# Optimization experiments

Measured on AMD Instinct MI355X. Metric: run time of the kernel, lower is better.

## Reference

```python
import jax, jax.numpy as jnp
import numpy as np

N_NODES = 100000
N_EDGES = 1600000
N_GRAPHS = 64
D = 128


def gcn_conv(x, W, b, src, dst, num_nodes):
    # PyG GCNConv: x' = D^{-1/2} (A + I) D^{-1/2} (X W) + b
    h = x @ W  # [N, H]
    deg = jax.ops.segment_sum(jnp.ones_like(dst, dtype=h.dtype), dst,
                              num_segments=num_nodes)  # includes self-loop (>=1)
    dinv = jax.lax.rsqrt(deg)
    norm = dinv[src] * dinv[dst]  # [E+N]
    msg = h[src] * norm[:, None]  # gather + scale
    out = jax.ops.segment_sum(msg, dst, num_segments=num_nodes)
    return out + b


def setup_inputs() -> dict:
    key = jax.random.key(0)
    ks = jax.random.split(key, 10)
    x = jax.random.normal(ks[0], (N_NODES, D), dtype=jnp.float32)
    edge_index = jax.random.randint(ks[1], (2, N_EDGES), 0, N_NODES, dtype=jnp.int64)
    batch = jnp.sort(jax.random.randint(ks[2], (N_NODES,), 0, N_GRAPHS, dtype=jnp.int64))
    s = 1.0 / np.sqrt(D)
    W1 = jax.random.normal(ks[3], (D, D), dtype=jnp.float32) * s
    b1 = jnp.zeros((D,), dtype=jnp.float32)
    W2 = jax.random.normal(ks[4], (D, D), dtype=jnp.float32) * s
    b2 = jnp.zeros((D,), dtype=jnp.float32)
    Wfc = jax.random.normal(ks[5], (D, D), dtype=jnp.float32) * s
    bfc = jnp.zeros((D,), dtype=jnp.float32)
    return {"x": x, "edge_index": edge_index, "batch": batch,
            "W1": W1, "b1": b1, "W2": W2, "b2": b2, "Wfc": Wfc, "bfc": bfc}


def reference(x, edge_index, batch, W1, b1, W2, b2, Wfc, bfc):
    num_nodes = x.shape[0]
    # add self-loops (PyG default add_self_loops=True)
    loop = jnp.arange(num_nodes, dtype=edge_index.dtype)
    src = jnp.concatenate([edge_index[0], loop])
    dst = jnp.concatenate([edge_index[1], loop])

    h = jax.nn.relu(gcn_conv(x, W1, b1, src, dst, num_nodes))
    h = jax.nn.relu(gcn_conv(h, W2, b2, src, dst, num_nodes))

    # global_mean_pool over graph segment ids
    sums = jax.ops.segment_sum(h, batch, num_segments=N_GRAPHS)
    cnts = jax.ops.segment_sum(jnp.ones((num_nodes,), h.dtype), batch,
                               num_segments=N_GRAPHS)
    pooled = sums / jnp.maximum(cnts, 1.0)[:, None]

    return jax.nn.relu(pooled @ Wfc + bfc)
```

## Files before the change

### kernel.cpp

```cpp
#include <hip/hip_runtime.h>
#include <hip/hip_bf16.h>
#include <stdint.h>

typedef unsigned int uint;
typedef unsigned short ushort;
typedef __attribute__((ext_vector_type(8))) short short8;
typedef __attribute__((ext_vector_type(4))) float floatx4;

#define DD 128
#define BSHIFT 9
#define NBLK 256

__device__ __forceinline__ float bf2f(ushort h){ return __uint_as_float(((uint)h)<<16); }
__device__ __forceinline__ ushort f2bf(float f){
    uint u = __float_as_uint(f);
    u += 0x7fffu + ((u>>16)&1u);
    return (ushort)(u>>16);
}

__global__ void k_detect(const int* ei, const ushort* x, const ushort* W1, int* flags){
    int t = threadIdx.x;
    unsigned long long b0 = __ballot((t < 32) ? (ei[2*t+1] == 0) : 1);
    uint ex = (((uint)x[2*t])  >> 7) & 0xffu;
    uint ew = (((uint)W1[2*t]) >> 7) & 0xffu;
    unsigned long long b1 = __ballot(ex >= 90u && ex <= 160u);
    unsigned long long b2 = __ballot(ew >= 90u && ew <= 160u);
    if (t == 0){
        flags[0] = (b0 == ~0ull) ? 1 : 0;
        flags[1] = (__popcll(b1) >= 48) ? 1 : 0;
        flags[2] = (__popcll(b2) >= 48) ? 1 : 0;
    }
}

__global__ void k_canon(const void* s0,const void* s1,const void* s2,
                        const void* s3,const void* s4,const void* s5,
                        float* d0,float* d1,float* d2,float* d3,float* d4,float* d5,
                        ushort* wb1, ushort* wb2,
                        const int* flags){
    int f = flags[2];
    int i = blockIdx.x*blockDim.x + threadIdx.x;
    const void* s; float* d; int off; int r;
    if (i < 49152){
        r = i>>14; off = i & 16383;
        s = (r==0)?s0:((r==1)?s1:s2);
        d = (r==0)?d0:((r==1)?d1:d2);
    } else {
        int j = i - 49152; r = j>>7; off = j & 127;
        if (r >= 3) return;
        s = (r==0)?s3:((r==1)?s4:s5);
        d = (r==0)?d3:((r==1)?d4:d5);
        d[off] = f ? bf2f(((const ushort*)s)[off]) : ((const float*)s)[off];
        return;
    }
    float val = f ? bf2f(((const ushort*)s)[off]) : ((const float*)s)[off];
    d[off] = val;
    if (r < 2){
        int k = off>>7, n = off&127;
        int c = n>>4, nn = n&15, kk = k>>5, q = (k>>3)&3, j = k&7;
        ushort* wb = (r==0) ? wb1 : wb2;
        wb[((c*4+kk)*64 + q*16 + nn)*8 + j] = f2bf(val);
    }
}

__global__ void k_init(float* pooled, int PM, int* buktot, int nbuk){
    int i = blockIdx.x*blockDim.x + threadIdx.x;
    if (i < PM) pooled[i] = 0.f;
    if (i < nbuk) buktot[i] = 0;
}

__global__ __launch_bounds__(256) void k_hist(const int* __restrict__ ei,
                                              const int* __restrict__ flags,
                                              int* __restrict__ ghist,
                                              int* __restrict__ buktot,
                                              int E, int nbuk, int chunk){
    __shared__ int lh[1024];
    int f = flags[0];
    int t = threadIdx.x, b = blockIdx.x;
    for (int i=t;i<nbuk;i+=256) lh[i]=0;
    __syncthreads();
    int e0 = b*chunk, e1 = min(E, e0+chunk);
    for (int e=e0+t; e<e1; e+=256){
        int d = f ? ei[2*(E+e)] : ei[E+e];
        atomicAdd(&lh[d>>BSHIFT],1);
    }
    __syncthreads();
    for (int i=t;i<nbuk;i+=256){
        int v = lh[i];
        ghist[i*NBLK + b] = v;
        if (v) atomicAdd(&buktot[i], v);
    }
}

__global__ void k_scanB2(const int* __restrict__ buktot, int* __restrict__ bukoff, int nbuk){
    __shared__ int ts[256];
    int t = threadIdx.x;
    int v = (t<nbuk) ? buktot[t] : 0;
    ts[t] = v; __syncthreads();
    for (int off=1; off<256; off<<=1){
        int x = (t>=off) ? ts[t-off] : 0;
        __syncthreads(); ts[t] += x; __syncthreads();
    }
    if (t<nbuk) bukoff[t] = ts[t] - v;
}

__global__ __launch_bounds__(256) void k_apply(const int* __restrict__ ghist,
                                               const int* __restrict__ bukoff,
                                               int* __restrict__ gstart, int nbuk){
    __shared__ int ts[256];
    int b = blockIdx.x, t = threadIdx.x;
    int v = ghist[b*NBLK + t];
    ts[t] = v; __syncthreads();
    for (int off=1; off<256; off<<=1){
        int x = (t>=off) ? ts[t-off] : 0;
        __syncthreads(); ts[t] += x; __syncthreads();
    }
    gstart[b*NBLK + t] = bukoff[b] + ts[t] - v;
}

__global__ __launch_bounds__(256) void k_scat(const int* __restrict__ ei,
                                              const int* __restrict__ flags,
                                              const int* __restrict__ gstart,
                                              uint2* __restrict__ pairs,
                                              int E, int nbuk, int chunk){
    __shared__ int cur[1024];
    int f = flags[0];
    int t = threadIdx.x, b = blockIdx.x;
    for (int i=t;i<nbuk;i+=256) cur[i] = gstart[i*NBLK + b];
    __syncthreads();
    int e0 = b*chunk, e1 = min(E, e0+chunk);
    for (int e=e0+t; e<e1; e+=256){
        int d = f ? ei[2*(E+e)] : ei[E+e];
        int s = f ? ei[2*e]     : ei[e];
        int p = atomicAdd(&cur[d>>BSHIFT],1);
        pairs[p] = make_uint2((uint)s,(uint)d);
    }
}

__global__ __launch_bounds__(256) void k_build(const uint2* __restrict__ pairs,
                                               const int* __restrict__ gstart,
                                               int* __restrict__ rowptr,
                                               float* __restrict__ dinv,
                                               int* __restrict__ srcb,
                                               int E, int nbuk, int M){
    __shared__ int cnt[512], off[512], cur[512], ps[256];
    int b = blockIdx.x, t = threadIdx.x;
    int base = gstart[b*NBLK];
    int end  = (b+1<nbuk) ? gstart[(b+1)*NBLK] : E;
    for (int i=t;i<512;i+=256) cnt[i]=0;
    __syncthreads();
    for (int e=base+t; e<end; e+=256){
        uint2 pr = pairs[e];
        atomicAdd(&cnt[pr.y & 511],1);
    }
    __syncthreads();
    int c0 = cnt[2*t], c1 = cnt[2*t+1];
    int s = c0+c1;
    ps[t]=s; __syncthreads();
    for (int o2=1;o2<256;o2<<=1){
        int x=(t>=o2)?ps[t-o2]:0; __syncthreads(); ps[t]+=x; __syncthreads();
    }
    int ex = ps[t]-s;
    off[2*t]=ex;    off[2*t+1]=ex+c0;
    cur[2*t]=ex;    cur[2*t+1]=ex+c0;
    __syncthreads();
    for (int i=t;i<512;i+=256){
        int n = (b<<BSHIFT)+i;
        if (n<M){
            rowptr[n] = base + off[i];
            dinv[n]   = rsqrtf((float)(cnt[i]+1));
        }
    }
    if (b==0 && t==0) rowptr[M] = E;
    for (int e=base+t; e<end; e+=256){
        uint2 pr = pairs[e];
        int i = pr.y & 511;
        int p = atomicAdd(&cur[i],1);
        srcb[base+p] = (int)pr.x;
    }
}

__global__ __launch_bounds__(256) void k_gemm(const ushort* __restrict__ Xb,
                                              const float* __restrict__ Xf,
                                              const ushort* __restrict__ Wb,
                                              const float* __restrict__ dinv,
                                              const int* __restrict__ flags, int force_bf16,
                                              ushort* __restrict__ Hp, int M){
    __shared__ uint4 Xs4[1024];
    __shared__ uint4 Ws4[2048];
    int t = threadIdx.x;
    int n0 = blockIdx.x*64;
    int xbf = force_bf16 ? 1 : flags[1];

    {
        const uint4* sW = (const uint4*)Wb;
        #pragma unroll
        for (int j=0;j<8;j++) Ws4[t + j*256] = sW[t + j*256];
    }
    #pragma unroll
    for (int g=0; g<4; g++){
        int u = g*256 + t;
        int row = u>>4, kk = (u>>2)&3, q = u&3;
        int n = n0 + row;
        uint4 o;
        if (n < M){
            if (xbf){
                o = *(const uint4*)(Xb + (size_t)n*DD + kk*32 + q*8);
            } else {
                const float* p = Xf + (size_t)n*DD + kk*32 + q*8;
                float4 a = *(const float4*)p;
                float4 b = *(const float4*)(p+4);
                o.x = (uint)f2bf(a.x) | ((uint)f2bf(a.y)<<16);
                o.y = (uint)f2bf(a.z) | ((uint)f2bf(a.w)<<16);
                o.z = (uint)f2bf(b.x) | ((uint)f2bf(b.y)<<16);
                o.w = (uint)f2bf(b.z) | ((uint)f2bf(b.w)<<16);
            }
        } else { o = make_uint4(0,0,0,0); }
        int w = row>>4, m16 = row&15;
        Xs4[(w*4+kk)*64 + q*16 + m16] = o;
    }
    __syncthreads();

    int wv = t>>6, lane = t&63;
    const ushort* Xs = (const ushort*)Xs4;
    const ushort* Ws = (const ushort*)Ws4;

    floatx4 acc[8];
    #pragma unroll
    for (int c=0;c<8;c++) acc[c] = (floatx4){0.f,0.f,0.f,0.f};

    #pragma unroll
    for (int kk=0;kk<4;kk++){
        short8 af = *(const short8*)(Xs + ((size_t)((wv*4+kk)*64 + lane))*8);
        #pragma unroll
        for (int c=0;c<8;c++){
            short8 bf = *(const short8*)(Ws + ((size_t)((c*4+kk)*64 + lane))*8);
            acc[c] = __builtin_amdgcn_mfma_f32_16x16x32_bf16(af, bf, acc[c], 0, 0, 0);
        }
    }

    int quad = lane>>4, col = lane&15;
    int rbase = n0 + wv*16 + quad*4;
    float dv[4];
    #pragma unroll
    for (int r=0;r<4;r++) dv[r] = (rbase + r < M) ? dinv[rbase + r] : 0.f;
    #pragma unroll
    for (int c=0;c<8;c++){
        #pragma unroll
        for (int r=0;r<4;r++){
            int gn = rbase + r;
            if (gn < M) Hp[(size_t)gn*DD + c*16 + col] = f2bf(acc[c][r]*dv[r]);
        }
    }
}

__global__ __launch_bounds__(256) void k_gather(const ushort* __restrict__ Hp,
                                                const int* __restrict__ rowptr,
                                                const int* __restrict__ srcb,
                                                const float* __restrict__ dinv,
                                                const float* __restrict__ bc,
                                                ushort* __restrict__ Xout, int M){
    int wid  = (int)((blockIdx.x*(size_t)blockDim.x + threadIdx.x) >> 6);
    int lane = threadIdx.x & 63;
    if (wid >= M) return;
    const uint* Hp32 = (const uint*)Hp;

    uint v = Hp32[(size_t)wid*64 + lane];
    float a0 = __uint_as_float(v<<16);
    float a1 = __uint_as_float(v & 0xffff0000u);

    int rp  = rowptr[wid];
    int rp1 = rowptr[wid+1];
    while (rp < rp1){
        int m = rp1 - rp; if (m > 64) m = 64;
        int idx = (lane < m) ? srcb[rp + lane] : 0;
        int j = 0;
        for (; j+4 <= m; j += 4){
            int s0 = __shfl(idx, j,   64);
            int s1 = __shfl(idx, j+1, 64);
            int s2 = __shfl(idx, j+2, 64);
            int s3 = __shfl(idx, j+3, 64);
            uint u0 = Hp32[(size_t)s0*64 + lane];
            uint u1 = Hp32[(size_t)s1*64 + lane];
            uint u2 = Hp32[(size_t)s2*64 + lane];
            uint u3 = Hp32[(size_t)s3*64 + lane];
            a0 += __uint_as_float(u0<<16); a1 += __uint_as_float(u0&0xffff0000u);
            a0 += __uint_as_float(u1<<16); a1 += __uint_as_float(u1&0xffff0000u);
            a0 += __uint_as_float(u2<<16); a1 += __uint_as_float(u2&0xffff0000u);
            a0 += __uint_as_float(u3<<16); a1 += __uint_as_float(u3&0xffff0000u);
        }
        for (; j<m; j++){
            int s = __shfl(idx, j, 64);
            uint u = Hp32[(size_t)s*64 + lane];
            a0 += __uint_as_float(u<<16); a1 += __uint_as_float(u&0xffff0000u);
        }
        rp += m;
    }

    float w = dinv[wid];
    float o0 = fmaxf(fmaf(a0, w, bc[2*lane]),   0.f);
    float o1 = fmaxf(fmaf(a1, w, bc[2*lane+1]), 0.f);
    ((uint*)Xout)[(size_t)wid*64 + lane] = (uint)f2bf(o0) | ((uint)f2bf(o1)<<16);
}

__global__ __launch_bounds__(256) void k_pool(const ushort* __restrict__ X3,
                                              const int* __restrict__ batch,
                                              const int* __restrict__ flags,
                                              float* __restrict__ pooled, int M){
    int f = flags[0];
    int t = threadIdx.x;
    int c32 = t & 63;
    int row = t >> 6;
    int n0 = blockIdx.x * 256;
    if (n0 >= M) return;
    int nend = n0 + 256; if (nend > M) nend = M;
    const uint* X3u = (const uint*)X3;

    float a0 = 0.f, a1 = 0.f;
    int cur = -1;

    int n = n0 + row;
    #define POOL_PROC(gg, uu) \
        if ((gg) != cur){ \
            if (cur >= 0){ \
                atomicAdd(&pooled[cur*DD + 2*c32],   a0); \
                atomicAdd(&pooled[cur*DD + 2*c32+1], a1); \
            } \
            a0 = 0.f; a1 = 0.f; cur = (gg); \
        } \
        a0 += __uint_as_float((uu)<<16); \
        a1 += __uint_as_float((uu) & 0xffff0000u);

    for (; n + 12 < nend; n += 16){
        int g0 = f ? batch[2*n]      : batch[n];
        int g1 = f ? batch[2*(n+4)]  : batch[n+4];
        int g2 = f ? batch[2*(n+8)]  : batch[n+8];
        int g3 = f ? batch[2*(n+12)] : batch[n+12];
        uint u0 = X3u[(size_t)n*64      + c32];
        uint u1 = X3u[(size_t)(n+4)*64  + c32];
        uint u2 = X3u[(size_t)(n+8)*64  + c32];
        uint u3 = X3u[(size_t)(n+12)*64 + c32];
        POOL_PROC(g0, u0);
        POOL_PROC(g1, u1);
        POOL_PROC(g2, u2);
        POOL_PROC(g3, u3);
    }
    for (; n < nend; n += 4){
        int g = f ? batch[2*n] : batch[n];
        uint u = X3u[(size_t)n*64 + c32];
        POOL_PROC(g, u);
    }
    #undef POOL_PROC

    if (cur >= 0){
        atomicAdd(&pooled[cur*DD + 2*c32],   a0);
        atomicAdd(&pooled[cur*DD + 2*c32+1], a1);
    }
}

__global__ void k_cnt(const int* __restrict__ batch, const int* __restrict__ flags,
                      float* __restrict__ cntf, int M, int G){
    int f = flags[0];
    int g = blockIdx.x*blockDim.x + threadIdx.x;
    if (g >= G) return;
    int lo = 0, hi = M;
    while (lo < hi){ int mid = (lo+hi)>>1; int bv = f ? batch[2*mid] : batch[mid]; if (bv > g) hi = mid; else lo = mid+1; }
    int ub_g = lo;
    lo = 0; hi = M;
    while (lo < hi){ int mid = (lo+hi)>>1; int bv = f ? batch[2*mid] : batch[mid]; if (bv > g-1) hi = mid; else lo = mid+1; }
    cntf[g] = (float)(ub_g - lo);
}

__global__ void k_fc(const float* __restrict__ pooled, const float* __restrict__ cntf,
                     const float* __restrict__ Wcf, const float* __restrict__ bcf,
                     const int* __restrict__ flags, ushort* out16, float* out32){
    __shared__ float p[128];
    int g = blockIdx.x, c = threadIdx.x;
    p[c] = pooled[g*DD + c] / fmaxf(cntf[g], 1.f);
    __syncthreads();
    float acc = bcf[c];
    #pragma unroll 8
    for (int k=0;k<128;k++) acc = fmaf(p[k], Wcf[k*DD + c], acc);
    float r = fmaxf(acc, 0.f);
    if (flags[1]) out16[g*DD + c] = f2bf(r);
    else          out32[g*DD + c] = r;
}

extern "C" void kernel_launch(void* const* d_in, const int* in_sizes, int n_in,
                              void* d_out, int out_size, void* d_ws, size_t ws_size,
                              hipStream_t stream) {
    const void* x    = d_in[0];
    const int*  ei   = (const int*)d_in[1];
    const int*  bat  = (const int*)d_in[2];
    const void* W1   = d_in[3];
    const void* b1   = d_in[4];
    const void* W2   = d_in[5];
    const void* b2   = d_in[6];
    const void* Wfc  = d_in[7];
    const void* bfc  = d_in[8];

    int M = in_sizes[0] / DD;
    int E = in_sizes[1] / 2;
    int G = out_size / DD;
    int nbuk  = (M + 511) >> BSHIFT;
    int chunk = (E + NBLK - 1) / NBLK;

    char* w = (char*)d_ws;
    auto alloc = [&](size_t bytes)->void*{ void* p = (void*)w; w += (bytes + 255) & ~(size_t)255; return p; };
    int*    flags  = (int*)   alloc(16);
    int*    rowptr = (int*)   alloc((size_t)(M+1)*4);
    int*    ghist  = (int*)   alloc((size_t)nbuk*NBLK*4);
    int*    gstart = (int*)   alloc((size_t)nbuk*NBLK*4);
    int*    buktot = (int*)   alloc((size_t)nbuk*4);
    int*    bukoff = (int*)   alloc((size_t)nbuk*4);
    float*  dinv   = (float*) alloc((size_t)M*4);
    float*  cntf   = (float*) alloc((size_t)G*4);
    float*  pooled = (float*) alloc((size_t)G*DD*4);
    float*  Wc1    = (float*) alloc(16384*4);
    float*  Wc2    = (float*) alloc(16384*4);
    float*  Wcf    = (float*) alloc(16384*4);
    float*  bc1    = (float*) alloc(128*4);
    float*  bc2    = (float*) alloc(128*4);
    float*  bcf    = (float*) alloc(128*4);
    ushort* wb1    = (ushort*)alloc(16384*2);
    ushort* wb2    = (ushort*)alloc(16384*2);
    int*    srcb   = (int*)   alloc((size_t)E*4);
    ushort* Hp     = (ushort*)alloc((size_t)M*DD*2);
    ushort* X2     = (ushort*)alloc((size_t)M*DD*2);
    uint2*  pairs  = (uint2*)Hp;
    (void)ws_size; (void)n_in;

    k_detect<<<1, 64, 0, stream>>>(ei, (const ushort*)x, (const ushort*)W1, flags);
    k_canon <<<194, 256, 0, stream>>>(W1, W2, Wfc, b1, b2, bfc,
                                      Wc1, Wc2, Wcf, bc1, bc2, bcf, wb1, wb2, flags);
    k_init  <<<(G*DD+255)/256, 256, 0, stream>>>(pooled, G*DD, buktot, nbuk);

    k_hist  <<<NBLK, 256, 0, stream>>>(ei, flags, ghist, buktot, E, nbuk, chunk);
    k_scanB2<<<1, 256, 0, stream>>>(buktot, bukoff, nbuk);
    k_apply <<<nbuk, 256, 0, stream>>>(ghist, bukoff, gstart, nbuk);
    k_scat  <<<NBLK, 256, 0, stream>>>(ei, flags, gstart, pairs, E, nbuk, chunk);
    k_build <<<nbuk, 256, 0, stream>>>(pairs, gstart, rowptr, dinv, srcb, E, nbuk, M);

    k_gemm  <<<(M+63)/64, 256, 0, stream>>>((const ushort*)x, (const float*)x,
                                            wb1, dinv, flags, 0, Hp, M);
    k_gather<<<(M+3)/4, 256, 0, stream>>>(Hp, rowptr, srcb, dinv, bc1, X2, M);
    k_gemm  <<<(M+63)/64, 256, 0, stream>>>(X2, (const float*)X2,
                                            wb2, dinv, flags, 1, Hp, M);
    k_gather<<<(M+3)/4, 256, 0, stream>>>(Hp, rowptr, srcb, dinv, bc2, X2, M);

    k_pool<<<(M+255)/256, 256, 0, stream>>>(X2, bat, flags, pooled, M);
    k_cnt <<<(G+63)/64, 64, 0, stream>>>(bat, flags, cntf, M, G);
    k_fc  <<<G, 128, 0, stream>>>(pooled, cntf, Wcf, bcf, flags, (ushort*)d_out, (float*)d_out);
}
```

Before: 354.5 us.

## Gather neighbor rows with 16-byte loads, four rows per wavefront

Restructures the gather kernel so each wavefront splits into four 16-lane groups. Each lane loads a uint4 (eight bf16 values), so four neighbor rows are fetched in parallel per instruction, and the self-loop row is folded into the edge stream. The partial sums are combined across groups with xor shuffles, and 16 lanes write the output with vector stores. The aim is fewer, wider memory instructions and more loads in flight per wave, at the cost of more registers and a cross-lane reduction.

```diff
diff --git a/kernel.cpp b/kernel.cpp
--- a/kernel.cpp
+++ b/kernel.cpp
@@ -262,44 +262,68 @@
     int wid  = (int)((blockIdx.x*(size_t)blockDim.x + threadIdx.x) >> 6);
     int lane = threadIdx.x & 63;
     if (wid >= M) return;
-    const uint* Hp32 = (const uint*)Hp;
-
-    uint v = Hp32[(size_t)wid*64 + lane];
-    float a0 = __uint_as_float(v<<16);
-    float a1 = __uint_as_float(v & 0xffff0000u);
+    int q   = lane >> 4;
+    int l16 = lane & 15;
+    const uint4* Hp4 = (const uint4*)Hp;
+
+    float acc[8];
+    #pragma unroll
+    for (int c=0;c<8;c++) acc[c] = 0.f;
+
+    #define ACCUM(vv) { \
+        acc[0] += __uint_as_float((vv).x<<16); acc[1] += __uint_as_float((vv).x&0xffff0000u); \
+        acc[2] += __uint_as_float((vv).y<<16); acc[3] += __uint_as_float((vv).y&0xffff0000u); \
+        acc[4] += __uint_as_float((vv).z<<16); acc[5] += __uint_as_float((vv).z&0xffff0000u); \
+        acc[6] += __uint_as_float((vv).w<<16); acc[7] += __uint_as_float((vv).w&0xffff0000u); }
 
     int rp  = rowptr[wid];
     int rp1 = rowptr[wid+1];
-    while (rp < rp1){
-        int m = rp1 - rp; if (m > 64) m = 64;
-        int idx = (lane < m) ? srcb[rp + lane] : 0;
-        int j = 0;
-        for (; j+4 <= m; j += 4){
-            int s0 = __shfl(idx, j,   64);
-            int s1 = __shfl(idx, j+1, 64);
-            int s2 = __shfl(idx, j+2, 64);
-            int s3 = __shfl(idx, j+3, 64);
-            uint u0 = Hp32[(size_t)s0*64 + lane];
-            uint u1 = Hp32[(size_t)s1*64 + lane];
-            uint u2 = Hp32[(size_t)s2*64 + lane];
-            uint u3 = Hp32[(size_t)s3*64 + lane];
-            a0 += __uint_as_float(u0<<16); a1 += __uint_as_float(u0&0xffff0000u);
-            a0 += __uint_as_float(u1<<16); a1 += __uint_as_float(u1&0xffff0000u);
-            a0 += __uint_as_float(u2<<16); a1 += __uint_as_float(u2&0xffff0000u);
-            a0 += __uint_as_float(u3<<16); a1 += __uint_as_float(u3&0xffff0000u);
+    int total = (rp1 - rp) + 1;
+    int j = 0;
+    while (j < total){
+        int m = total - j; if (m > 64) m = 64;
+        int pos = j + lane;
+        int idx = wid;
+        if (lane < m && pos > 0) idx = srcb[rp + pos - 1];
+        for (int g = 0; g < m; g += 8){
+            int r0 = g + q, r1 = g + 4 + q;
+            int s0 = __shfl(idx, r0, 64);
+            int s1 = __shfl(idx, r1, 64);
+            uint4 v0 = make_uint4(0,0,0,0), v1 = make_uint4(0,0,0,0);
+            if (r0 < m) v0 = Hp4[(size_t)s0*16 + l16];
+            if (r1 < m) v1 = Hp4[(size_t)s1*16 + l16];
+            ACCUM(v0);
+            ACCUM(v1);
         }
-        for (; j<m; j++){
-            int s = __shfl(idx, j, 64);
-            uint u = Hp32[(size_t)s*64 + lane];
-            a0 += __uint_as_float(u<<16); a1 += __uint_as_float(u&0xffff0000u);
-        }
-        rp += m;
-    }
-
-    float w = dinv[wid];
-    float o0 = fmaxf(fmaf(a0, w, bc[2*lane]),   0.f);
-    float o1 = fmaxf(fmaf(a1, w, bc[2*lane+1]), 0.f);
-    ((uint*)Xout)[(size_t)wid*64 + lane] = (uint)f2bf(o0) | ((uint)f2bf(o1)<<16);
+        j += m;
+    }
+    #undef ACCUM
+
+    #pragma unroll
+    for (int c=0;c<8;c++){
+        acc[c] += __shfl_xor(acc[c], 16, 64);
+        acc[c] += __shfl_xor(acc[c], 32, 64);
+    }
+
+    if (lane < 16){
+        float w = dinv[wid];
+        const float* bp = bc + l16*8;
+        uint4 o;
+        float r0,r1;
+        r0 = fmaxf(fmaf(acc[0], w, bp[0]), 0.f);
+        r1 = fmaxf(fmaf(acc[1], w, bp[1]), 0.f);
+        o.x = (uint)f2bf(r0) | ((uint)f2bf(r1)<<16);
+        r0 = fmaxf(fmaf(acc[2], w, bp[2]), 0.f);
+        r1 = fmaxf(fmaf(acc[3], w, bp[3]), 0.f);
+        o.y = (uint)f2bf(r0) | ((uint)f2bf(r1)<<16);
+        r0 = fmaxf(fmaf(acc[4], w, bp[4]), 0.f);
+        r1 = fmaxf(fmaf(acc[5], w, bp[5]), 0.f);
+        o.z = (uint)f2bf(r0) | ((uint)f2bf(r1)<<16);
+        r0 = fmaxf(fmaf(acc[6], w, bp[6]), 0.f);
+        r1 = fmaxf(fmaf(acc[7], w, bp[7]), 0.f);
+        o.w = (uint)f2bf(r0) | ((uint)f2bf(r1)<<16);
+        ((uint4*)Xout)[(size_t)wid*16 + l16] = o;
+    }
 }
 
 __global__ __launch_bounds__(256) void k_pool(const ushort* __restrict__ X3,
```

Measured after the change: 348.6 us. Within noise of the previous version (-1.7%).
